# Kernel tuning notes

Measured on AMD Instinct MI355X. Metric: run time of the kernel, lower is better.

Reference implementation:

```python
import jax, jax.numpy as jnp
import numpy as np

D_MODEL = 1024
H = 16
D_K = D_MODEL // H
B = 4
S = 2048


def setup_inputs() -> dict:
    key = jax.random.key(0)
    ks = jax.random.split(key, 7)
    q = jax.random.normal(ks[0], (B, S, D_MODEL), dtype=jnp.float32)
    k = jax.random.normal(ks[1], (B, S, D_MODEL), dtype=jnp.float32)
    v = jax.random.normal(ks[2], (B, S, D_MODEL), dtype=jnp.float32)
    # nn.Linear weights have shape (out_features, in_features); y = x @ W.T
    scale = 1.0 / np.sqrt(D_MODEL)
    w_q = jax.random.normal(ks[3], (D_MODEL, D_MODEL), dtype=jnp.float32) * scale
    w_k = jax.random.normal(ks[4], (D_MODEL, D_MODEL), dtype=jnp.float32) * scale
    w_v = jax.random.normal(ks[5], (D_MODEL, D_MODEL), dtype=jnp.float32) * scale
    w_o = jax.random.normal(ks[6], (D_MODEL, D_MODEL), dtype=jnp.float32) * scale
    mask = jnp.ones((1, 1, S, S), dtype=bool)  # broadcasts over [B,H,S,S]
    return {"q": q, "k": k, "v": v, "w_q": w_q, "w_k": w_k, "w_v": w_v,
            "w_o": w_o, "mask": mask}


def reference(q, k, v, w_q, w_k, w_v, w_o, mask):
    # projections (nn.Linear, no bias): x @ W.T
    query = jnp.einsum('bsd,ed->bse', q, w_q)
    key_p = jnp.einsum('bsd,ed->bse', k, w_k)
    value = jnp.einsum('bsd,ed->bse', v, w_v)
    # split heads: [B,S,D] -> [B,H,S,d_k]
    query = query.reshape(B, S, H, D_K).transpose(0, 2, 1, 3)
    key_p = key_p.reshape(B, S, H, D_K).transpose(0, 2, 1, 3)
    value = value.reshape(B, S, H, D_K).transpose(0, 2, 1, 3)
    # scaled dot-product attention (explicit softmax, as in source)
    scores = jnp.einsum('bhqd,bhkd->bhqk', query, key_p) / jnp.sqrt(
        jnp.asarray(D_K, dtype=query.dtype))
    scores = jnp.where(mask, scores, jnp.asarray(-1e9, dtype=scores.dtype))
    weights = jax.nn.softmax(scores, axis=-1)
    ctx = jnp.einsum('bhqk,bhkd->bhqd', weights, value)
    # merge heads and output projection
    ctx = ctx.transpose(0, 2, 1, 3).reshape(B, S, D_MODEL)
    return jnp.einsum('bsd,ed->bse', ctx, w_o)
```

## Files before the change

kernel.cpp:

```cpp
#include <hip/hip_runtime.h>
#include <hip/hip_bf16.h>
#include <stdint.h>
#include <math.h>

#define DM 1024
#define SS 2048
#define HH 16

typedef unsigned short u16;
typedef __attribute__((ext_vector_type(8))) short short8;
typedef __attribute__((ext_vector_type(4))) float f32x4;
typedef __attribute__((ext_vector_type(4))) unsigned short u16x4;

#define C_SCALE 0.18033688011112042f

__device__ __forceinline__ u16 f2bf(float f) {
    union { float f; uint32_t u; } v; v.f = f;
    uint32_t r = v.u + 0x7FFFu + ((v.u >> 16) & 1u);
    return (u16)(r >> 16);
}

__device__ __forceinline__ void async_cp16(const void* g, void* l) {
    __builtin_amdgcn_global_load_lds(
        reinterpret_cast<const __attribute__((address_space(1))) unsigned int*>(
            reinterpret_cast<uintptr_t>(g)),
        reinterpret_cast<__attribute__((address_space(3))) unsigned int*>(
            reinterpret_cast<uintptr_t>(l)),
        16, 0, 0);
}

__global__ __launch_bounds__(256) void cast_bf16(const float* __restrict__ in,
                                                 u16* __restrict__ out, int n4)
{
    int i = blockIdx.x * 256 + threadIdx.x;
    if (i < n4) {
        float4 v = ((const float4*)in)[i];
        u16x4 p = { f2bf(v.x), f2bf(v.y), f2bf(v.z), f2bf(v.w) };
        ((u16x4*)out)[i] = p;
    }
}

template<int MODE>
__global__ __launch_bounds__(256) void gemm_bt(const u16* __restrict__ A,
                                               const u16* __restrict__ B,
                                               void* __restrict__ C)
{
    __shared__ char sm[32768];
    const uint32_t t = threadIdx.x;
    const uint32_t l = t & 63u, w = t >> 6;
    uint32_t id = blockIdx.x;
    id = (id & 7u) * 64u + (id >> 3);
    const uint32_t bm = id >> 3, bn = id & 7u;
    const uint32_t wr = w >> 1, wc = w & 1u;

    const uint32_t q15 = l & 15u, G = l >> 4, xq = q15 & 7u;
    const uint32_t vbg0 = q15 * 128u + ((G ^ (xq & 3u)) << 4) + ((xq >> 2) << 6);
    const uint32_t vA0 = wr * 8192u + vbg0,          vA1 = vA0 ^ 64u;
    const uint32_t vB0 = 16384u + wc * 8192u + vbg0, vB1 = vB0 ^ 64u;

    uint32_t La[4];
    const u16* aP[4];
    const u16* bP[4];
    #pragma unroll
    for (uint32_t i = 0; i < 4; ++i) {
        La[i] = (i * 256u + t) * 16u;
        const uint32_t r = La[i] >> 7;
        const uint32_t c8 = ((La[i] >> 4) & 7u) ^ (r & 7u);
        aP[i] = A + (size_t)(bm * 128u + r) * DM + c8 * 8u;
        bP[i] = B + (size_t)(bn * 128u + r) * DM + c8 * 8u;
    }

    f32x4 acc[4][4] = {};

    for (uint32_t k0 = 0; k0 < 1024; k0 += 64) {
        __syncthreads();
        #pragma unroll
        for (uint32_t i = 0; i < 4; ++i) async_cp16(aP[i] + k0, sm + La[i]);
        #pragma unroll
        for (uint32_t i = 0; i < 4; ++i) async_cp16(bP[i] + k0, sm + 16384 + La[i]);
        __syncthreads();

        #pragma unroll
        for (uint32_t kk = 0; kk < 2; ++kk) {
            const uint32_t va = kk ? vA1 : vA0;
            const uint32_t vb = kk ? vB1 : vB0;
            short8 a[4], b[4];
            #pragma unroll
            for (uint32_t m = 0; m < 4; ++m)
                a[m] = *(const short8*)(sm + va + m * 2048u);
            #pragma unroll
            for (uint32_t n = 0; n < 4; ++n)
                b[n] = *(const short8*)(sm + vb + n * 2048u);
            #pragma unroll
            for (uint32_t m = 0; m < 4; ++m)
                #pragma unroll
                for (uint32_t n = 0; n < 4; ++n)
                    acc[m][n] = __builtin_amdgcn_mfma_f32_16x16x32_bf16(
                        a[m], b[n], acc[m][n], 0, 0, 0);
        }
    }

    #pragma unroll
    for (uint32_t m = 0; m < 4; ++m) {
        #pragma unroll
        for (uint32_t n = 0; n < 4; ++n) {
            const uint32_t rmb = bm * 128u + wr * 64u + m * 16u + G * 4u;
            const uint32_t cn  = bn * 128u + wc * 64u + n * 16u + q15;
            if (MODE == 0 || MODE == 3) {
                const float sc = (MODE == 3) ? C_SCALE : 1.0f;
                #pragma unroll
                for (uint32_t g = 0; g < 4; ++g)
                    ((u16*)C)[(size_t)(rmb + g) * DM + cn] = f2bf(acc[m][n][g] * sc);
            } else if (MODE == 1) {
                const uint32_t b_ = rmb >> 11, s0 = rmb & 2047u;
                u16x4 pk;
                #pragma unroll
                for (uint32_t g = 0; g < 4; ++g) pk[g] = f2bf(acc[m][n][g]);
                *(u16x4*)((u16*)C + (size_t)(b_ * 1024u + cn) * 2048u + s0) = pk;
            } else {
                #pragma unroll
                for (uint32_t g = 0; g < 4; ++g)
                    ((float*)C)[(size_t)(rmb + g) * DM + cn] = acc[m][n][g];
            }
        }
    }
}

__global__ __launch_bounds__(256) void attn_mfma(const u16* __restrict__ Q,
                                                 const u16* __restrict__ K,
                                                 const u16* __restrict__ Vt,
                                                 u16* __restrict__ ctx)
{
    __shared__ char sm[51200];
    const uint32_t t = threadIdx.x, l = t & 63u, w = t >> 6;
    uint32_t id = blockIdx.x;
    id = (id & 7u) * 128u + (id >> 3);
    const uint32_t qt = id & 15u, h = (id >> 4) & 15u, b = id >> 8;

    const uint32_t q15 = l & 15u, G = l >> 4, xq = q15 & 7u;

    const uint32_t vb0 = q15 * 128u + ((G ^ (xq & 3u)) << 4) + ((xq >> 2) << 6);
    const uint32_t vb1 = vb0 ^ 64u;
    const uint32_t vbPw = w * 4608u + q15 * 144u + G * 8u;
    const uint32_t vbPr = w * 4608u + q15 * 144u + G * 16u;

    short8 qf[2][2];
    #pragma unroll
    for (uint32_t qb = 0; qb < 2; ++qb) {
        const size_t qrow = (size_t)(b * 2048u + qt * 128u + w * 32u + qb * 16u + q15);
        const uint32_t col = h * 64u + (G << 3);
        qf[qb][0] = *(const short8*)(Q + qrow * DM + col);
        qf[qb][1] = *(const short8*)(Q + qrow * DM + col + 32u);
    }

    short8 ones;
    #pragma unroll
    for (int i = 0; i < 8; ++i) ones[i] = (short)0x3F80;
    const f32x4 ZV = {0.f, 0.f, 0.f, 0.f};

    f32x4 o[2][4] = {};
    f32x4 osum[2] = {};

    uint32_t Ls[2];
    const u16* kcur[2];
    const u16* vcur[2];
    {
        const size_t kbase = (size_t)b * 2048u * DM + h * 64u;
        const size_t vbase = (size_t)((b * 16u + h) * 64u) * 2048u;
        #pragma unroll
        for (uint32_t i = 0; i < 2; ++i) {
            Ls[i] = (i * 256u + t) * 16u;
            const uint32_t r = Ls[i] >> 7;
            const uint32_t c8 = ((Ls[i] >> 4) & 7u) ^ (r & 7u);
            const u16* k0p = K  + kbase + (size_t)r * DM    + c8 * 8u;
            const u16* v0p = Vt + vbase + (size_t)r * 2048u + c8 * 8u;
            async_cp16(k0p, sm + Ls[i]);
            async_cp16(v0p, sm + 8192 + Ls[i]);
            kcur[i] = k0p + (size_t)64u * DM;
            vcur[i] = v0p + 64u;
        }
    }

#define ATTN_STEP(BCc, BNc, STAGE)                                             \
    {                                                                          \
        if (STAGE) {                                                           \
            _Pragma("unroll")                                                  \
            for (uint32_t i = 0; i < 2; ++i) {                                 \
                async_cp16(kcur[i], sm + (BNc) + Ls[i]);                       \
                async_cp16(vcur[i], sm + (BNc) + 8192u + Ls[i]);               \
                kcur[i] += (size_t)64u * DM;                                   \
                vcur[i] += 64u;                                                \
            }                                                                  \
            asm volatile("s_waitcnt vmcnt(4)" ::: "memory");                   \
        } else {                                                               \
            asm volatile("s_waitcnt vmcnt(0)" ::: "memory");                   \
        }                                                                      \
        __builtin_amdgcn_s_barrier();                                          \
        __builtin_amdgcn_sched_barrier(0);                                     \
        f32x4 s[2][4];                                                         \
        __builtin_amdgcn_s_setprio(1);                                         \
        _Pragma("unroll")                                                      \
        for (uint32_t mf = 0; mf < 4; ++mf) {                                  \
            short8 kf0 = *(const short8*)(sm + (BCc) + vb0 + mf * 2048u);      \
            short8 kf1 = *(const short8*)(sm + (BCc) + vb1 + mf * 2048u);      \
            _Pragma("unroll")                                                  \
            for (uint32_t qb = 0; qb < 2; ++qb) {                              \
                s[qb][mf] = __builtin_amdgcn_mfma_f32_16x16x32_bf16(           \
                    kf1, qf[qb][1],                                            \
                    __builtin_amdgcn_mfma_f32_16x16x32_bf16(                   \
                        kf0, qf[qb][0], ZV, 0, 0, 0),                          \
                    0, 0, 0);                                                  \
            }                                                                  \
        }                                                                      \
        __builtin_amdgcn_s_setprio(0);                                         \
        _Pragma("unroll")                                                      \
        for (uint32_t qb = 0; qb < 2; ++qb) {                                  \
            _Pragma("unroll")                                                  \
            for (uint32_t mf = 0; mf < 4; ++mf) {                              \
                float p0 = __builtin_amdgcn_exp2f(s[qb][mf][0]);               \
                float p1 = __builtin_amdgcn_exp2f(s[qb][mf][1]);               \
                float p2 = __builtin_amdgcn_exp2f(s[qb][mf][2]);               \
                float p3 = __builtin_amdgcn_exp2f(s[qb][mf][3]);               \
                union { u16x4 v; struct { __hip_bfloat162 lo, hi; } b; } pk;   \
                pk.b.lo = __float22bfloat162_rn(make_float2(p0, p1));          \
                pk.b.hi = __float22bfloat162_rn(make_float2(p2, p3));          \
                *(u16x4*)(sm + 32768u + vbPw + qb * 2304u + mf * 32u) = pk.v;  \
            }                                                                  \
        }                                                                      \
        _Pragma("unroll")                                                      \
        for (uint32_t kk = 0; kk < 2; ++kk) {                                  \
            const uint32_t vv = (kk ? vb1 : vb0) + 8192u;                      \
            short8 vf[4];                                                      \
            _Pragma("unroll")                                                  \
            for (uint32_t d = 0; d < 4; ++d)                                   \
                vf[d] = *(const short8*)(sm + (BCc) + vv + d * 2048u);         \
            __builtin_amdgcn_s_setprio(1);                                     \
            _Pragma("unroll")                                                  \
            for (uint32_t qb = 0; qb < 2; ++qb) {                              \
                short8 pf = *(const short8*)(sm + 32768u + vbPr +              \
                                             qb * 2304u + kk * 64u);           \
                _Pragma("unroll")                                              \
                for (uint32_t d = 0; d < 4; ++d)                               \
                    o[qb][d] = __builtin_amdgcn_mfma_f32_16x16x32_bf16(        \
                        pf, vf[d], o[qb][d], 0, 0, 0);                         \
                osum[qb] = __builtin_amdgcn_mfma_f32_16x16x32_bf16(            \
                    pf, ones, osum[qb], 0, 0, 0);                              \
            }                                                                  \
            __builtin_amdgcn_s_setprio(0);                                     \
        }                                                                      \
        asm volatile("s_waitcnt lgkmcnt(0)" ::: "memory");                     \
        __builtin_amdgcn_s_barrier();                                          \
        __builtin_amdgcn_sched_barrier(0);                                     \
    }

    for (uint32_t it = 0; it < 15; ++it) {
        ATTN_STEP(0u, 16384u, true)
        ATTN_STEP(16384u, 0u, true)
    }
    ATTN_STEP(0u, 16384u, true)
    ATTN_STEP(16384u, 0u, false)

#undef ATTN_STEP

    #pragma unroll
    for (uint32_t qb = 0; qb < 2; ++qb) {
        float inv[4];
        #pragma unroll
        for (int g = 0; g < 4; ++g) inv[g] = 1.0f / osum[qb][g];
        #pragma unroll
        for (uint32_t d = 0; d < 4; ++d)
            #pragma unroll
            for (int g = 0; g < 4; ++g) {
                const uint32_t srow = qt * 128u + w * 32u + qb * 16u + G * 4u + (uint32_t)g;
                const uint32_t col  = h * 64u + d * 16u + q15;
                ctx[(size_t)(b * 2048u + srow) * DM + col] = f2bf(o[qb][d][g] * inv[g]);
            }
    }
}

extern "C" void kernel_launch(void* const* d_in, const int* in_sizes, int n_in,
                              void* d_out, int out_size, void* d_ws, size_t ws_size,
                              hipStream_t stream)
{
    const float* q  = (const float*)d_in[0];
    const float* k  = (const float*)d_in[1];
    const float* v  = (const float*)d_in[2];
    const float* wq = (const float*)d_in[3];
    const float* wk = (const float*)d_in[4];
    const float* wv = (const float*)d_in[5];
    const float* wo = (const float*)d_in[6];

    const size_t SZ = (size_t)4 * 2048 * 1024;
    const size_t WZ = (size_t)1024 * 1024;
    u16* qb  = (u16*)d_ws;
    u16* Qp  = qb  + SZ;
    u16* Kp  = Qp  + SZ;
    u16* Vtp = Kp  + SZ;
    u16* wqb = Vtp + SZ;
    u16* wkb = wqb + WZ;
    u16* wvb = wkb + WZ;
    u16* wob = wvb + WZ;

    cast_bf16<<<1024, 256, 0, stream>>>(wq, wqb, (int)(WZ / 4));
    cast_bf16<<<1024, 256, 0, stream>>>(wk, wkb, (int)(WZ / 4));
    cast_bf16<<<1024, 256, 0, stream>>>(wv, wvb, (int)(WZ / 4));
    cast_bf16<<<1024, 256, 0, stream>>>(wo, wob, (int)(WZ / 4));

    cast_bf16<<<8192, 256, 0, stream>>>(q, qb, (int)(SZ / 4));
    gemm_bt<3><<<512, 256, 0, stream>>>(qb, wqb, Qp);
    cast_bf16<<<8192, 256, 0, stream>>>(k, qb, (int)(SZ / 4));
    gemm_bt<0><<<512, 256, 0, stream>>>(qb, wkb, Kp);
    cast_bf16<<<8192, 256, 0, stream>>>(v, qb, (int)(SZ / 4));
    gemm_bt<1><<<512, 256, 0, stream>>>(qb, wvb, Vtp);

    attn_mfma<<<1024, 256, 0, stream>>>(Qp, Kp, Vtp, qb);

    gemm_bt<2><<<512, 256, 0, stream>>>(qb, wob, d_out);
}
```

Baseline: 216.8 us.

## Double attention block to 8 waves sharing K/V tiles; fuse weight casts

The attention kernel now runs 512-thread blocks covering 256 query rows. Each K/V tile staged in LDS is reused by twice as many waves, and each thread issues one async copy per tile instead of two. This halves global/L2 K/V traffic per query and changes the grid to 512 blocks, which may fill the CUs more evenly. The cost is larger LDS per block (more P scratch), which can limit occupancy. The four weight-cast launches are also merged into one kernel to cut launch overhead.

New measurement: 194.7 us. 10.2% less time.

```diff
diff --git a/kernel.cpp b/kernel.cpp
--- a/kernel.cpp
+++ b/kernel.cpp
@@ -38,6 +38,24 @@
         u16x4 p = { f2bf(v.x), f2bf(v.y), f2bf(v.z), f2bf(v.w) };
         ((u16x4*)out)[i] = p;
     }
+}
+
+__global__ __launch_bounds__(256) void cast_w4(const float* __restrict__ w0,
+                                               const float* __restrict__ w1,
+                                               const float* __restrict__ w2,
+                                               const float* __restrict__ w3,
+                                               u16* __restrict__ o0,
+                                               u16* __restrict__ o1,
+                                               u16* __restrict__ o2,
+                                               u16* __restrict__ o3)
+{
+    const uint32_t which = blockIdx.x >> 10;
+    const uint32_t i = (blockIdx.x & 1023u) * 256u + threadIdx.x;
+    const float* in = which == 0 ? w0 : which == 1 ? w1 : which == 2 ? w2 : w3;
+    u16* out = which == 0 ? o0 : which == 1 ? o1 : which == 2 ? o2 : o3;
+    float4 v = ((const float4*)in)[i];
+    u16x4 p = { f2bf(v.x), f2bf(v.y), f2bf(v.z), f2bf(v.w) };
+    ((u16x4*)out)[i] = p;
 }
 
 template<int MODE>
@@ -126,16 +144,16 @@
     }
 }
 
-__global__ __launch_bounds__(256) void attn_mfma(const u16* __restrict__ Q,
+__global__ __launch_bounds__(512) void attn_mfma(const u16* __restrict__ Q,
                                                  const u16* __restrict__ K,
                                                  const u16* __restrict__ Vt,
                                                  u16* __restrict__ ctx)
 {
-    __shared__ char sm[51200];
+    __shared__ char sm[69632];
     const uint32_t t = threadIdx.x, l = t & 63u, w = t >> 6;
     uint32_t id = blockIdx.x;
-    id = (id & 7u) * 128u + (id >> 3);
-    const uint32_t qt = id & 15u, h = (id >> 4) & 15u, b = id >> 8;
+    id = (id & 7u) * 64u + (id >> 3);
+    const uint32_t qt = id & 7u, h = (id >> 3) & 15u, b = id >> 7;
 
     const uint32_t q15 = l & 15u, G = l >> 4, xq = q15 & 7u;
 
@@ -147,7 +165,7 @@
     short8 qf[2][2];
     #pragma unroll
     for (uint32_t qb = 0; qb < 2; ++qb) {
-        const size_t qrow = (size_t)(b * 2048u + qt * 128u + w * 32u + qb * 16u + q15);
+        const size_t qrow = (size_t)(b * 2048u + qt * 256u + w * 32u + qb * 16u + q15);
         const uint32_t col = h * 64u + (G << 3);
         qf[qb][0] = *(const short8*)(Q + qrow * DM + col);
         qf[qb][1] = *(const short8*)(Q + qrow * DM + col + 32u);
@@ -161,37 +179,30 @@
     f32x4 o[2][4] = {};
     f32x4 osum[2] = {};
 
-    uint32_t Ls[2];
-    const u16* kcur[2];
-    const u16* vcur[2];
+    const uint32_t Ls = t * 16u;
+    const u16* kcur;
+    const u16* vcur;
     {
         const size_t kbase = (size_t)b * 2048u * DM + h * 64u;
         const size_t vbase = (size_t)((b * 16u + h) * 64u) * 2048u;
-        #pragma unroll
-        for (uint32_t i = 0; i < 2; ++i) {
-            Ls[i] = (i * 256u + t) * 16u;
-            const uint32_t r = Ls[i] >> 7;
-            const uint32_t c8 = ((Ls[i] >> 4) & 7u) ^ (r & 7u);
-            const u16* k0p = K  + kbase + (size_t)r * DM    + c8 * 8u;
-            const u16* v0p = Vt + vbase + (size_t)r * 2048u + c8 * 8u;
-            async_cp16(k0p, sm + Ls[i]);
-            async_cp16(v0p, sm + 8192 + Ls[i]);
-            kcur[i] = k0p + (size_t)64u * DM;
-            vcur[i] = v0p + 64u;
-        }
+        const uint32_t r = Ls >> 7;
+        const uint32_t c8 = ((Ls >> 4) & 7u) ^ (r & 7u);
+        const u16* k0p = K  + kbase + (size_t)r * DM    + c8 * 8u;
+        const u16* v0p = Vt + vbase + (size_t)r * 2048u + c8 * 8u;
+        async_cp16(k0p, sm + Ls);
+        async_cp16(v0p, sm + 8192 + Ls);
+        kcur = k0p + (size_t)64u * DM;
+        vcur = v0p + 64u;
     }
 
 #define ATTN_STEP(BCc, BNc, STAGE)                                             \
     {                                                                          \
         if (STAGE) {                                                           \
-            _Pragma("unroll")                                                  \
-            for (uint32_t i = 0; i < 2; ++i) {                                 \
-                async_cp16(kcur[i], sm + (BNc) + Ls[i]);                       \
-                async_cp16(vcur[i], sm + (BNc) + 8192u + Ls[i]);               \
-                kcur[i] += (size_t)64u * DM;                                   \
-                vcur[i] += 64u;                                                \
-            }                                                                  \
-            asm volatile("s_waitcnt vmcnt(4)" ::: "memory");                   \
+            async_cp16(kcur, sm + (BNc) + Ls);                                 \
+            async_cp16(vcur, sm + (BNc) + 8192u + Ls);                         \
+            kcur += (size_t)64u * DM;                                          \
+            vcur += 64u;                                                       \
+            asm volatile("s_waitcnt vmcnt(2)" ::: "memory");                   \
         } else {                                                               \
             asm volatile("s_waitcnt vmcnt(0)" ::: "memory");                   \
         }                                                                      \
@@ -271,7 +282,7 @@
         for (uint32_t d = 0; d < 4; ++d)
             #pragma unroll
             for (int g = 0; g < 4; ++g) {
-                const uint32_t srow = qt * 128u + w * 32u + qb * 16u + G * 4u + (uint32_t)g;
+                const uint32_t srow = qt * 256u + w * 32u + qb * 16u + G * 4u + (uint32_t)g;
                 const uint32_t col  = h * 64u + d * 16u + q15;
                 ctx[(size_t)(b * 2048u + srow) * DM + col] = f2bf(o[qb][d][g] * inv[g]);
             }
@@ -301,10 +312,7 @@
     u16* wvb = wkb + WZ;
     u16* wob = wvb + WZ;
 
-    cast_bf16<<<1024, 256, 0, stream>>>(wq, wqb, (int)(WZ / 4));
-    cast_bf16<<<1024, 256, 0, stream>>>(wk, wkb, (int)(WZ / 4));
-    cast_bf16<<<1024, 256, 0, stream>>>(wv, wvb, (int)(WZ / 4));
-    cast_bf16<<<1024, 256, 0, stream>>>(wo, wob, (int)(WZ / 4));
+    cast_w4<<<4096, 256, 0, stream>>>(wq, wk, wv, wo, wqb, wkb, wvb, wob);
 
     cast_bf16<<<8192, 256, 0, stream>>>(q, qb, (int)(SZ / 4));
     gemm_bt<3><<<512, 256, 0, stream>>>(qb, wqb, Qp);
@@ -313,7 +321,7 @@
     cast_bf16<<<8192, 256, 0, stream>>>(v, qb, (int)(SZ / 4));
     gemm_bt<1><<<512, 256, 0, stream>>>(qb, wvb, Vtp);
 
-    attn_mfma<<<1024, 256, 0, stream>>>(Qp, Kp, Vtp, qb);
+    attn_mfma<<<512, 512, 0, stream>>>(Qp, Kp, Vtp, qb);
 
     gemm_bt<2><<<512, 256, 0, stream>>>(qb, wob, d_out);
 }
```
